# Kernel optimization log

Measured on AMD Instinct MI355X. Metric: run time of the kernel, lower is better.

The kernel has to match this reference:

```python
import jax, jax.numpy as jnp
import numpy as np

N_NODES = 100000
N_EDGES = 1000000
D_FEAT = 64


def setup_inputs() -> dict:
    key = jax.random.key(0)
    k1, k2, k3 = jax.random.split(key, 3)
    features = jax.random.normal(k1, (N_NODES, D_FEAT), dtype=jnp.float32)
    src = jax.random.randint(k2, (N_EDGES,), 0, N_NODES, dtype=jnp.int64)
    dst = jax.random.randint(k3, (N_EDGES,), 0, N_NODES, dtype=jnp.int64)
    return {"features": features, "src": src, "dst": dst}


def reference(features, src, dst):
    # DGL update_all(copy_u('h','m'), sum('m','h')):
    # out[v] = sum_{(u,v) in E} features[u]
    msgs = features[src]  # [E, D] gather of source node features
    h = jax.ops.segment_sum(msgs, dst, num_segments=N_NODES)  # [N, D] scatter-add
    return h
```

## Files before the change

### kernel.cpp

```cpp
#include <hip/hip_runtime.h>


#define N_NODES   100000
#define N_EDGES   1000000
#define D_FEAT    64
#define NPB       128
#define NPB_SHIFT 7
#define NB        782
#define PAD       32
#define EPB       8192
#define MAXP      4096

__global__ void zero_ints_kernel(int* __restrict__ p, int n) {
    int i = blockIdx.x * blockDim.x + threadIdx.x;
    if (i < n) p[i] = 0;
}

__global__ __launch_bounds__(512) void hist_kernel(const int* __restrict__ dst,
                                                   int* __restrict__ gcounts, int n) {
    __shared__ int cnt[NB];
    for (int i = threadIdx.x; i < NB; i += 512) cnt[i] = 0;
    __syncthreads();
    int base = blockIdx.x * EPB + threadIdx.x * 4;
#pragma unroll
    for (int step = 0; step < 4; ++step) {
        int idx = base + step * 2048;
        if (idx < n) {
            int4 d = *reinterpret_cast<const int4*>(dst + idx);
            atomicAdd(&cnt[d.x >> NPB_SHIFT], 1);
            atomicAdd(&cnt[d.y >> NPB_SHIFT], 1);
            atomicAdd(&cnt[d.z >> NPB_SHIFT], 1);
            atomicAdd(&cnt[d.w >> NPB_SHIFT], 1);
        }
    }
    __syncthreads();
    for (int b = threadIdx.x; b < NB; b += 512)
        if (cnt[b]) atomicAdd(&gcounts[b * PAD], cnt[b]);
}

__global__ __launch_bounds__(1024) void scan_kernel(const int* __restrict__ gcounts,
                                                    int* __restrict__ bases,
                                                    int* __restrict__ gcursor, int n_edges) {
    __shared__ int lds[1024];
    int t = threadIdx.x;
    int v = (t < NB) ? gcounts[t * PAD] : 0;
    lds[t] = v;
    __syncthreads();
    for (int off = 1; off < 1024; off <<= 1) {
        int u = (t >= off) ? lds[t - off] : 0;
        __syncthreads();
        lds[t] += u;
        __syncthreads();
    }
    if (t < NB) { int b = lds[t] - v; bases[t] = b; gcursor[t * PAD] = b; }
    if (t == 0) bases[NB] = n_edges;
}

__global__ __launch_bounds__(512) void partition_kernel(const int* __restrict__ src,
                                                        const int* __restrict__ dst,
                                                        int* __restrict__ gcursor,
                                                        int* __restrict__ pairs, int n) {
    __shared__ int cnt[NB];
    __shared__ int lbase[NB];
    for (int i = threadIdx.x; i < NB; i += 512) cnt[i] = 0;
    __syncthreads();

    int base = blockIdx.x * EPB + threadIdx.x * 4;
    int4 s[4], d[4];
    bool valid[4];
#pragma unroll
    for (int step = 0; step < 4; ++step) {
        int idx = base + step * 2048;
        valid[step] = (idx < n);
        if (valid[step]) {
            s[step] = *reinterpret_cast<const int4*>(src + idx);
            d[step] = *reinterpret_cast<const int4*>(dst + idx);
            atomicAdd(&cnt[d[step].x >> NPB_SHIFT], 1);
            atomicAdd(&cnt[d[step].y >> NPB_SHIFT], 1);
            atomicAdd(&cnt[d[step].z >> NPB_SHIFT], 1);
            atomicAdd(&cnt[d[step].w >> NPB_SHIFT], 1);
        }
    }
    __syncthreads();
    for (int b = threadIdx.x; b < NB; b += 512) {
        int c = cnt[b];
        lbase[b] = c ? atomicAdd(&gcursor[b * PAD], c) : 0;
    }
    __syncthreads();
    for (int b = threadIdx.x; b < NB; b += 512) cnt[b] = 0;
    __syncthreads();
#pragma unroll
    for (int step = 0; step < 4; ++step) {
        if (valid[step]) {
            int b, p;
            b = d[step].x >> NPB_SHIFT; p = atomicAdd(&cnt[b], 1); pairs[lbase[b] + p] = (s[step].x << NPB_SHIFT) | (d[step].x & (NPB - 1));
            b = d[step].y >> NPB_SHIFT; p = atomicAdd(&cnt[b], 1); pairs[lbase[b] + p] = (s[step].y << NPB_SHIFT) | (d[step].y & (NPB - 1));
            b = d[step].z >> NPB_SHIFT; p = atomicAdd(&cnt[b], 1); pairs[lbase[b] + p] = (s[step].z << NPB_SHIFT) | (d[step].z & (NPB - 1));
            b = d[step].w >> NPB_SHIFT; p = atomicAdd(&cnt[b], 1); pairs[lbase[b] + p] = (s[step].w << NPB_SHIFT) | (d[step].w & (NPB - 1));
        }
    }
}

__global__ __launch_bounds__(512) void gather_kernel(const float* __restrict__ feat,
                                                     const int* __restrict__ bases,
                                                     const int* __restrict__ pairs,
                                                     float* __restrict__ out,
                                                     int n_nodes) {
    __shared__ int pbuf[MAXP];
    __shared__ int sorted[MAXP];
    __shared__ int deg[NPB];
    __shared__ int sc[NPB];
    __shared__ int start[NPB + 1];
    __shared__ int cur[NPB];

    int b = blockIdx.x, t = threadIdx.x;
    int lane = t & 63, wave = t >> 6;
    int lo = bases[b], hi = bases[b + 1];
    int node0 = b * NPB;

    bool first = true;
    for (int c = lo; c < hi || first; c += MAXP) {
        int n = hi - c;
        if (n > MAXP) n = MAXP;
        if (n < 0) n = 0;

        if (t < NPB) deg[t] = 0;
        __syncthreads();
        for (int i = t; i < n; i += 512) {
            int p = pairs[c + i];
            pbuf[i] = p;
            atomicAdd(&deg[p & (NPB - 1)], 1);
        }
        __syncthreads();
        if (t < NPB) sc[t] = deg[t];
        __syncthreads();
        for (int off = 1; off < NPB; off <<= 1) {
            int u = (t < NPB && t >= off) ? sc[t - off] : 0;
            __syncthreads();
            if (t < NPB) sc[t] += u;
            __syncthreads();
        }
        if (t < NPB) { start[t + 1] = sc[t]; cur[t] = sc[t] - deg[t]; }
        if (t == 0) start[0] = 0;
        __syncthreads();
        for (int i = t; i < n; i += 512) {
            int p = pbuf[i];
            int r = p & (NPB - 1);
            int pos = atomicAdd(&cur[r], 1);
            sorted[pos] = p >> NPB_SHIFT;
        }
        __syncthreads();

        for (int r = wave; r < NPB; r += 8) {
            int s0 = start[r], e0 = start[r + 1];
            float acc = 0.f;
            int i = s0;
            for (; i + 3 < e0; i += 4) {
                int i0 = sorted[i], i1 = sorted[i + 1], i2 = sorted[i + 2], i3 = sorted[i + 3];
                float v0 = feat[(size_t)i0 * D_FEAT + lane];
                float v1 = feat[(size_t)i1 * D_FEAT + lane];
                float v2 = feat[(size_t)i2 * D_FEAT + lane];
                float v3 = feat[(size_t)i3 * D_FEAT + lane];
                acc += v0 + v1 + v2 + v3;
            }
            for (; i < e0; ++i) acc += feat[(size_t)sorted[i] * D_FEAT + lane];

            int node = node0 + r;
            if (node < n_nodes) {
                float* o = out + (size_t)node * D_FEAT + lane;
                if (first) *o = acc;
                else atomicAdd(o, acc);
            }
        }
        first = false;
        __syncthreads();
    }
}

extern "C" void kernel_launch(void* const* d_in, const int* in_sizes, int n_in,
                              void* d_out, int out_size, void* d_ws, size_t ws_size,
                              hipStream_t stream) {
    const float* feat = (const float*)d_in[0];
    const int*   src  = (const int*)d_in[1];
    const int*   dst  = (const int*)d_in[2];
    float*       out  = (float*)d_out;

    const int n_edges = in_sizes[1];

    int* gcounts = (int*)d_ws;
    int* gcursor = gcounts + NB * PAD;
    int* bases   = gcursor + NB * PAD;
    int* pairs   = bases + NB + 1;

    int nzero = NB * PAD;
    zero_ints_kernel<<<(nzero + 255) / 256, 256, 0, stream>>>(gcounts, nzero);

    int pblocks = (n_edges + EPB - 1) / EPB;
    hist_kernel<<<pblocks, 512, 0, stream>>>(dst, gcounts, n_edges);
    scan_kernel<<<1, 1024, 0, stream>>>(gcounts, bases, gcursor, n_edges);
    partition_kernel<<<pblocks, 512, 0, stream>>>(src, dst, gcursor, pairs, n_edges);
    gather_kernel<<<NB, 512, 0, stream>>>(feat, bases, pairs, out, N_NODES);
}
```

Baseline: 76.36 us.

## Split gather blocks per node half and use float4 multi-edge loads per wave

The gather kernel now runs two 256-thread blocks per 128-node bucket, each owning 64 destination nodes and filtering the bucket's pairs by half. Each wave processes four edges at once, with 16 lanes per edge doing float4 loads, and then reduces the partial sums across lane groups with xor shuffles. The aim is more blocks for occupancy, wider loads and more memory-level parallelism per wave. In exchange, each block reads every pair in the bucket twice (once to count, once to scatter), so pair reads double. Only 16 lanes store each output row.

```diff
diff --git a/kernel.cpp b/kernel.cpp
--- a/kernel.cpp
+++ b/kernel.cpp
@@ -9,7 +9,7 @@
 #define NB        782
 #define PAD       32
 #define EPB       8192
-#define MAXP      4096
+#define CH        2048
 
 __global__ void zero_ints_kernel(int* __restrict__ p, int n) {
     int i = blockIdx.x * blockDim.x + threadIdx.x;
@@ -101,75 +101,84 @@
     }
 }
 
-__global__ __launch_bounds__(512) void gather_kernel(const float* __restrict__ feat,
+__global__ __launch_bounds__(256) void gather_kernel(const float* __restrict__ feat,
                                                      const int* __restrict__ bases,
                                                      const int* __restrict__ pairs,
                                                      float* __restrict__ out,
                                                      int n_nodes) {
-    __shared__ int pbuf[MAXP];
-    __shared__ int sorted[MAXP];
-    __shared__ int deg[NPB];
-    __shared__ int sc[NPB];
-    __shared__ int start[NPB + 1];
-    __shared__ int cur[NPB];
-
-    int b = blockIdx.x, t = threadIdx.x;
+    __shared__ int sorted[CH];
+    __shared__ int deg[64];
+    __shared__ int sc[64];
+    __shared__ int start[65];
+    __shared__ int cur[64];
+
+    int bb   = blockIdx.x >> 1;
+    int half = blockIdx.x & 1;
+    int t = threadIdx.x;
     int lane = t & 63, wave = t >> 6;
-    int lo = bases[b], hi = bases[b + 1];
-    int node0 = b * NPB;
+    int g = lane >> 4, l16 = lane & 15;
+    int lo = bases[bb], hi = bases[bb + 1];
+    int node0 = bb * NPB + half * 64;
 
     bool first = true;
-    for (int c = lo; c < hi || first; c += MAXP) {
+    for (int c = lo; c < hi || first; c += CH) {
         int n = hi - c;
-        if (n > MAXP) n = MAXP;
+        if (n > CH) n = CH;
         if (n < 0) n = 0;
 
-        if (t < NPB) deg[t] = 0;
-        __syncthreads();
-        for (int i = t; i < n; i += 512) {
+        if (t < 64) deg[t] = 0;
+        __syncthreads();
+        for (int i = t; i < n; i += 256) {
+            int r = pairs[c + i] & (NPB - 1);
+            if ((r >> 6) == half) atomicAdd(&deg[r & 63], 1);
+        }
+        __syncthreads();
+        if (t < 64) sc[t] = deg[t];
+        __syncthreads();
+        for (int off = 1; off < 64; off <<= 1) {
+            int u = (t < 64 && t >= off) ? sc[t - off] : 0;
+            __syncthreads();
+            if (t < 64) sc[t] += u;
+            __syncthreads();
+        }
+        if (t < 64) { start[t + 1] = sc[t]; cur[t] = sc[t] - deg[t]; }
+        if (t == 0) start[0] = 0;
+        __syncthreads();
+        for (int i = t; i < n; i += 256) {
             int p = pairs[c + i];
-            pbuf[i] = p;
-            atomicAdd(&deg[p & (NPB - 1)], 1);
-        }
-        __syncthreads();
-        if (t < NPB) sc[t] = deg[t];
-        __syncthreads();
-        for (int off = 1; off < NPB; off <<= 1) {
-            int u = (t < NPB && t >= off) ? sc[t - off] : 0;
-            __syncthreads();
-            if (t < NPB) sc[t] += u;
-            __syncthreads();
-        }
-        if (t < NPB) { start[t + 1] = sc[t]; cur[t] = sc[t] - deg[t]; }
-        if (t == 0) start[0] = 0;
-        __syncthreads();
-        for (int i = t; i < n; i += 512) {
-            int p = pbuf[i];
             int r = p & (NPB - 1);
-            int pos = atomicAdd(&cur[r], 1);
-            sorted[pos] = p >> NPB_SHIFT;
-        }
-        __syncthreads();
-
-        for (int r = wave; r < NPB; r += 8) {
+            if ((r >> 6) == half) {
+                int pos = atomicAdd(&cur[r & 63], 1);
+                sorted[pos] = p >> NPB_SHIFT;
+            }
+        }
+        __syncthreads();
+
+        for (int r = wave; r < 64; r += 4) {
             int s0 = start[r], e0 = start[r + 1];
-            float acc = 0.f;
-            int i = s0;
-            for (; i + 3 < e0; i += 4) {
-                int i0 = sorted[i], i1 = sorted[i + 1], i2 = sorted[i + 2], i3 = sorted[i + 3];
-                float v0 = feat[(size_t)i0 * D_FEAT + lane];
-                float v1 = feat[(size_t)i1 * D_FEAT + lane];
-                float v2 = feat[(size_t)i2 * D_FEAT + lane];
-                float v3 = feat[(size_t)i3 * D_FEAT + lane];
-                acc += v0 + v1 + v2 + v3;
+            float4 acc = {0.f, 0.f, 0.f, 0.f};
+            for (int i = s0; i < e0; i += 4) {
+                if (g < e0 - i) {
+                    int sn = sorted[i + g];
+                    const float4 v = *reinterpret_cast<const float4*>(
+                        feat + (size_t)sn * D_FEAT + l16 * 4);
+                    acc.x += v.x; acc.y += v.y; acc.z += v.z; acc.w += v.w;
+                }
             }
-            for (; i < e0; ++i) acc += feat[(size_t)sorted[i] * D_FEAT + lane];
+            acc.x += __shfl_xor(acc.x, 16); acc.y += __shfl_xor(acc.y, 16);
+            acc.z += __shfl_xor(acc.z, 16); acc.w += __shfl_xor(acc.w, 16);
+            acc.x += __shfl_xor(acc.x, 32); acc.y += __shfl_xor(acc.y, 32);
+            acc.z += __shfl_xor(acc.z, 32); acc.w += __shfl_xor(acc.w, 32);
 
             int node = node0 + r;
-            if (node < n_nodes) {
-                float* o = out + (size_t)node * D_FEAT + lane;
-                if (first) *o = acc;
-                else atomicAdd(o, acc);
+            if (node < n_nodes && lane < 16) {
+                float* o = out + (size_t)node * D_FEAT + l16 * 4;
+                if (first) {
+                    *reinterpret_cast<float4*>(o) = acc;
+                } else {
+                    atomicAdd(o + 0, acc.x); atomicAdd(o + 1, acc.y);
+                    atomicAdd(o + 2, acc.z); atomicAdd(o + 3, acc.w);
+                }
             }
         }
         first = false;
@@ -199,5 +208,5 @@
     hist_kernel<<<pblocks, 512, 0, stream>>>(dst, gcounts, n_edges);
     scan_kernel<<<1, 1024, 0, stream>>>(gcounts, bases, gcursor, n_edges);
     partition_kernel<<<pblocks, 512, 0, stream>>>(src, dst, gcursor, pairs, n_edges);
-    gather_kernel<<<NB, 512, 0, stream>>>(feat, bases, pairs, out, N_NODES);
-}
+    gather_kernel<<<NB * 2, 256, 0, stream>>>(feat, bases, pairs, out, N_NODES);
+}
```

Measured after the change: 78.12 us. 1.02x slower.
